# Performance work log

Hardware: AMD Instinct MI355X
Metric: run time of the kernel (lower is better)

Reference implementation:

```python
import jax, jax.numpy as jnp
import numpy as np

NEG_SLOPE = 0.01  # F.leaky_relu default
EPS = 1e-6


def setup_inputs() -> dict:
    key = jax.random.key(0)
    k1, k2, k3, k4 = jax.random.split(key, 4)
    N, E, IN, OUT = 100000, 1600000, 128, 64
    x = jax.random.normal(k1, (N, IN), dtype=jnp.float32)
    W = jax.random.normal(k2, (OUT, IN), dtype=jnp.float32) * (1.0 / np.sqrt(IN))
    a = jax.random.uniform(k3, (2 * OUT,), dtype=jnp.float32)  # uniform [0,1) as in init
    edge_index = jax.random.randint(k4, (2, E), 0, N, dtype=jnp.int64)
    return {"x": x, "W": W, "a": a, "edge_index": edge_index}


def reference(x, W, a, edge_index):
    N = x.shape[0]
    out_f = W.shape[0]
    # add self loops: append (i, i) for every node
    loops = jnp.arange(N, dtype=edge_index.dtype)
    ei = jnp.concatenate([edge_index, jnp.stack([loops, loops])], axis=1)
    src, dst = ei[0], ei[1]

    messages = x @ W.T                      # [N, out]
    h_src = messages[src]                   # [E', out]
    h_dst = messages[dst]                   # [E', out]

    # e = cat([h_dst, h_src]) . a  == h_dst.a[:out] + h_src.a[out:]
    e = h_dst @ a[:out_f] + h_src @ a[out_f:]
    e = jnp.where(e >= 0, e, NEG_SLOPE * e)  # leaky_relu
    w = jnp.exp(e)                           # unnormalized edge weights

    denom = jax.ops.segment_sum(w, dst, num_segments=N)                     # [N]
    agg = jax.ops.segment_sum(h_src * w[:, None], dst, num_segments=N)      # [N, out]
    return agg / jnp.clip(denom, EPS)[:, None]
```

## Files before the change

kernel.cpp:

```cpp
#include <hip/hip_runtime.h>
#include <hip/hip_bf16.h>

#define IN_F 128
#define OUT_F 64
#define NEG 0.01f
#define LDSP 132
#define WTP  68

#define BUCKET_N 256
#define EPB 8192
#define CAP 48
#define MAXB 512
#define MAXSLAB 512
#define CMAXIT 32

__device__ __forceinline__ float leaky_exp(float e) {
    e = (e >= 0.f) ? e : NEG * e;
    return expf(e);
}

__device__ __forceinline__ float b2f(unsigned int v) { return __uint_as_float(v); }

__global__ __launch_bounds__(256) void gemm_msg_kernel(
    const float* __restrict__ x, const float* __restrict__ W,
    const float* __restrict__ a,
    __hip_bfloat16* __restrict__ msg, float2* __restrict__ ab, int N)
{
    __shared__ float xs[64 * LDSP];
    __shared__ float Wt[IN_F * WTP];
    const int tid = threadIdx.x;
    const int base = blockIdx.x * 64;

#pragma unroll
    for (int t = 0; t < 8; ++t) {
        int i = tid + t * 256;
        int o = i & 63;
        int k4 = i >> 6;
        float4 wv = ((const float4*)W)[o * (IN_F / 4) + k4];
        Wt[(k4 * 4 + 0) * WTP + o] = wv.x;
        Wt[(k4 * 4 + 1) * WTP + o] = wv.y;
        Wt[(k4 * 4 + 2) * WTP + o] = wv.z;
        Wt[(k4 * 4 + 3) * WTP + o] = wv.w;
    }
#pragma unroll
    for (int t = 0; t < 8; ++t) {
        int i = tid + t * 256;
        int r = i >> 5, k4 = i & 31;
        int row = base + r;
        float4 xv = make_float4(0.f, 0.f, 0.f, 0.f);
        if (row < N) xv = ((const float4*)x)[(size_t)row * (IN_F / 4) + k4];
        *(float4*)&xs[r * LDSP + k4 * 4] = xv;
    }
    __syncthreads();

    const int tx = tid & 15;
    const int ty = tid >> 4;
    const float* xrow = &xs[(ty * 4) * LDSP];

    float acc[4][4] = {};
    for (int k = 0; k < IN_F; k += 4) {
        float xq[4][4], wq[4][4];
#pragma unroll
        for (int i = 0; i < 4; ++i)
            *(float4*)xq[i] = *(const float4*)&xrow[i * LDSP + k];
#pragma unroll
        for (int j = 0; j < 4; ++j)
            *(float4*)wq[j] = *(const float4*)&Wt[(k + j) * WTP + tx * 4];
#pragma unroll
        for (int ri = 0; ri < 4; ++ri)
#pragma unroll
            for (int ci = 0; ci < 4; ++ci) {
                acc[ri][ci] += xq[ri][0] * wq[0][ci];
                acc[ri][ci] += xq[ri][1] * wq[1][ci];
                acc[ri][ci] += xq[ri][2] * wq[2][ci];
                acc[ri][ci] += xq[ri][3] * wq[3][ci];
            }
    }

    float a_lo[4], a_hi[4];
#pragma unroll
    for (int ci = 0; ci < 4; ++ci) {
        a_lo[ci] = a[tx * 4 + ci];
        a_hi[ci] = a[OUT_F + tx * 4 + ci];
    }

#pragma unroll
    for (int ri = 0; ri < 4; ++ri) {
        int row = base + ty * 4 + ri;
        if (row < N) {
            union { ushort4 u; __hip_bfloat16 h[4]; } pk;
            pk.h[0] = __float2bfloat16(acc[ri][0]);
            pk.h[1] = __float2bfloat16(acc[ri][1]);
            pk.h[2] = __float2bfloat16(acc[ri][2]);
            pk.h[3] = __float2bfloat16(acc[ri][3]);
            *(ushort4*)&msg[(size_t)row * OUT_F + tx * 4] = pk.u;
        }
        float pa = acc[ri][0] * a_lo[0] + acc[ri][1] * a_lo[1] +
                   acc[ri][2] * a_lo[2] + acc[ri][3] * a_lo[3];
        float pb = acc[ri][0] * a_hi[0] + acc[ri][1] * a_hi[1] +
                   acc[ri][2] * a_hi[2] + acc[ri][3] * a_hi[3];
#pragma unroll
        for (int off = 1; off < 16; off <<= 1) {
            pa += __shfl_xor(pa, off);
            pb += __shfl_xor(pb, off);
        }
        if (tx == 0 && row < N) ab[row] = make_float2(pa, pb);
    }
}

__global__ __launch_bounds__(512) void partition_kernel(
    const int* __restrict__ src, const int* __restrict__ dst,
    int* __restrict__ counts, unsigned int* __restrict__ cells,
    int* __restrict__ bucket_tot, int E, int B, int NBLKP)
{
    __shared__ int cnt_s[MAXB];
    for (int i = threadIdx.x; i < B; i += 512) cnt_s[i] = 0;
    __syncthreads();

    const size_t pbase = (size_t)blockIdx.x * B;

#pragma unroll
    for (int u = 0; u < 4; ++u) {
        const int i4 = blockIdx.x * 2048 + u * 512 + threadIdx.x;
        const int e0 = i4 * 4;
        if (e0 + 3 < E) {
            int4 s4 = ((const int4*)src)[i4];
            int4 d4 = ((const int4*)dst)[i4];
            int b0 = d4.x >> 8, b1 = d4.y >> 8, b2 = d4.z >> 8, b3 = d4.w >> 8;
            int r0 = atomicAdd(&cnt_s[b0], 1);
            int r1 = atomicAdd(&cnt_s[b1], 1);
            int r2 = atomicAdd(&cnt_s[b2], 1);
            int r3 = atomicAdd(&cnt_s[b3], 1);
            if (r0 < CAP) cells[(pbase + b0) * CAP + r0] =
                (unsigned)s4.x | ((unsigned)(d4.x & 255) << 20);
            if (r1 < CAP) cells[(pbase + b1) * CAP + r1] =
                (unsigned)s4.y | ((unsigned)(d4.y & 255) << 20);
            if (r2 < CAP) cells[(pbase + b2) * CAP + r2] =
                (unsigned)s4.z | ((unsigned)(d4.z & 255) << 20);
            if (r3 < CAP) cells[(pbase + b3) * CAP + r3] =
                (unsigned)s4.w | ((unsigned)(d4.w & 255) << 20);
        } else {
            for (int e = e0; e < E && e < e0 + 4; ++e) {
                int s = src[e], d = dst[e];
                int b = d >> 8;
                int r = atomicAdd(&cnt_s[b], 1);
                if (r < CAP) cells[(pbase + b) * CAP + r] =
                    (unsigned)s | ((unsigned)(d & 255) << 20);
            }
        }
    }
    __syncthreads();
    for (int i = threadIdx.x; i < B; i += 512) {
        int c = min(cnt_s[i], CAP);
        counts[(size_t)i * NBLKP + blockIdx.x] = c;
        atomicAdd(&bucket_tot[i], c);
    }
}

__global__ __launch_bounds__(512) void bucket_scan_kernel(
    const int* __restrict__ bucket_tot, int* __restrict__ bucket_base,
    int* __restrict__ offs, int N, int B)
{
    __shared__ int tmp[512];
    const int t = threadIdx.x;
    int v = 0;
    if (t < B) {
        int nodes = N - t * BUCKET_N;
        nodes = max(0, min(BUCKET_N, nodes));
        v = bucket_tot[t] + nodes;
    }
    tmp[t] = v;
    __syncthreads();
#pragma unroll
    for (int d = 1; d < 512; d <<= 1) {
        int add = (t >= d) ? tmp[t - d] : 0;
        __syncthreads();
        tmp[t] += add;
        __syncthreads();
    }
    if (t < B) bucket_base[t] = tmp[t] - v;
    if (t == 511) offs[N] = tmp[511];
}

__global__ __launch_bounds__(512) void compact_kernel(
    const int* __restrict__ counts, const unsigned int* __restrict__ cells,
    const int* __restrict__ bucket_base, const float2* __restrict__ ab,
    int* __restrict__ offs, int2* __restrict__ edges,
    int N, int B, int NBLK, int NBLKP)
{
    __shared__ int cnt_l[MAXSLAB];
    __shared__ int hist[BUCKET_N];
    __shared__ int scan_s[BUCKET_N];
    __shared__ int cursor[BUCKET_N];
    __shared__ float alpha_s[BUCKET_N];
    const int b = blockIdx.x;
    const int tid = threadIdx.x;
    const int wave = tid >> 6, lane = tid & 63;

    for (int i = tid; i < NBLK; i += 512) cnt_l[i] = counts[(size_t)b * NBLKP + i];
    float2 myab = make_float2(0.f, 0.f);
    if (tid < BUCKET_N) {
        int g = b * BUCKET_N + tid;
        bool valid = (g < N);
        hist[tid] = valid ? 1 : 0;
        if (valid) myab = ab[g];
        alpha_s[tid] = myab.x;
    }
    __syncthreads();

    unsigned cell_c[CMAXIT];
#pragma unroll
    for (int it = 0; it < CMAXIT; ++it) {
        int sl = wave + it * 8;
        unsigned v = 0xFFFFFFFFu;
        if (sl < NBLK) {
            int c = cnt_l[sl];
            if (lane < c) {
                v = cells[((size_t)sl * B + b) * CAP + lane];
                atomicAdd(&hist[v >> 20], 1);
            }
        }
        cell_c[it] = v;
    }
    for (int sl = wave + CMAXIT * 8; sl < NBLK; sl += 8) {
        int c = cnt_l[sl];
        if (lane < c) {
            unsigned v = cells[((size_t)sl * B + b) * CAP + lane];
            atomicAdd(&hist[v >> 20], 1);
        }
    }
    __syncthreads();

    int hv = 0;
    if (tid < BUCKET_N) { hv = hist[tid]; scan_s[tid] = hv; }
    __syncthreads();
#pragma unroll
    for (int d = 1; d < BUCKET_N; d <<= 1) {
        int add = (tid < BUCKET_N && tid >= d) ? scan_s[tid - d] : 0;
        __syncthreads();
        if (tid < BUCKET_N) scan_s[tid] += add;
        __syncthreads();
    }
    const int gbase = bucket_base[b];
    if (tid < BUCKET_N) {
        int excl = scan_s[tid] - hv;
        int g = b * BUCKET_N + tid;
        if (g < N) {
            offs[g] = gbase + excl;
            float wself = leaky_exp(myab.x + myab.y);
            edges[gbase + excl] = make_int2(g, __float_as_int(wself));
            cursor[tid] = excl + 1;
        }
    }
    __syncthreads();

#pragma unroll
    for (int it = 0; it < CMAXIT; ++it) {
        unsigned v = cell_c[it];
        if (v != 0xFFFFFFFFu) {
            int s = v & 0xFFFFF;
            int l = (v >> 20) & 255;
            float w = leaky_exp(alpha_s[l] + ab[s].y);
            int pos = atomicAdd(&cursor[l], 1);
            edges[gbase + pos] = make_int2(s, __float_as_int(w));
        }
    }
    for (int sl = wave + CMAXIT * 8; sl < NBLK; sl += 8) {
        int c = cnt_l[sl];
        if (lane < c) {
            unsigned v = cells[((size_t)sl * B + b) * CAP + lane];
            int s = v & 0xFFFFF;
            int l = (v >> 20) & 255;
            float w = leaky_exp(alpha_s[l] + ab[s].y);
            int pos = atomicAdd(&cursor[l], 1);
            edges[gbase + pos] = make_int2(s, __float_as_int(w));
        }
    }
}

__global__ __launch_bounds__(256) void aggregate_kernel(
    const int* __restrict__ offs, const int2* __restrict__ edges,
    const __hip_bfloat16* __restrict__ msg,
    float* __restrict__ out, int N)
{
    const int node = blockIdx.x * 4 + (threadIdx.x >> 6);
    if (node >= N) return;
    const int lane = threadIdx.x & 63;
    const int g = lane & 15;
    const int u = lane >> 4;

    const unsigned short* msp = (const unsigned short*)msg;

    float acc0 = 0.f, acc1 = 0.f, acc2 = 0.f, acc3 = 0.f, den = 0.f;

    const int st = offs[node], en = offs[node + 1];

    int idx = st + u;
    int2 e = edges[min(idx, en - 1)];
    for (int j = st; j < en; j += 4) {
        const int nidx = idx + 4;
        const int2 enx = edges[min(nidx, en - 1)];
        const float w = (idx < en) ? __int_as_float(e.y) : 0.f;
        const ushort4 mv = *(const ushort4*)&msp[(size_t)e.x * OUT_F + 4 * g];
        acc0 += w * b2f((unsigned)mv.x << 16);
        acc1 += w * b2f((unsigned)mv.y << 16);
        acc2 += w * b2f((unsigned)mv.z << 16);
        acc3 += w * b2f((unsigned)mv.w << 16);
        den  += w;
        idx = nidx;
        e = enx;
    }

#pragma unroll
    for (int off = 16; off <= 32; off <<= 1) {
        acc0 += __shfl_xor(acc0, off);
        acc1 += __shfl_xor(acc1, off);
        acc2 += __shfl_xor(acc2, off);
        acc3 += __shfl_xor(acc3, off);
        den  += __shfl_xor(den, off);
    }

    if (lane < 16) {
        float dn = 1.f / fmaxf(den, 1e-6f);
        *(float4*)&out[(size_t)node * OUT_F + 4 * lane] =
            make_float4(acc0 * dn, acc1 * dn, acc2 * dn, acc3 * dn);
    }
}

extern "C" void kernel_launch(void* const* d_in, const int* in_sizes, int n_in,
                              void* d_out, int out_size, void* d_ws, size_t ws_size,
                              hipStream_t stream) {
    const float* x  = (const float*)d_in[0];
    const float* W  = (const float*)d_in[1];
    const float* a  = (const float*)d_in[2];
    const int*   ei = (const int*)d_in[3];
    float* out = (float*)d_out;

    const int IN = in_sizes[1] / OUT_F;
    const int N  = in_sizes[0] / IN;
    const int E  = in_sizes[3] / 2;
    const int B  = (N + BUCKET_N - 1) / BUCKET_N;
    const int NBLK  = (E + EPB - 1) / EPB;
    const int NBLKP = (NBLK + 3) & ~3;

    auto align16 = [](size_t v) { return (v + 15) & ~(size_t)15; };
    char* p = (char*)d_ws;
    __hip_bfloat16* msg = (__hip_bfloat16*)p; p += align16((size_t)N * OUT_F * 2);
    float2* ab    = (float2*)p; p += align16((size_t)N * 8);
    int*   counts = (int*)p;   p += align16((size_t)B * NBLKP * 4);
    unsigned int* cells = (unsigned int*)p; p += align16((size_t)NBLK * B * CAP * 4);
    int*   btot   = (int*)p;   p += align16((size_t)B * 4);
    int*   bbase  = (int*)p;   p += align16((size_t)B * 4);
    int*   offs   = (int*)p;   p += align16((size_t)(N + 1) * 4);
    int2*  edges  = (int2*)p;  p += align16((size_t)(E + N) * 8);

    const int* esrc = ei;
    const int* edst = ei + E;

    hipMemsetAsync(btot, 0, (size_t)B * 4, stream);

    gemm_msg_kernel<<<(N + 63) / 64, 256, 0, stream>>>(x, W, a, msg, ab, N);
    partition_kernel<<<NBLK, 512, 0, stream>>>(esrc, edst, counts, cells,
                                               btot, E, B, NBLKP);
    bucket_scan_kernel<<<1, 512, 0, stream>>>(btot, bbase, offs, N, B);
    compact_kernel<<<B, 512, 0, stream>>>(counts, cells, bbase, ab,
                                          offs, edges, N, B, NBLK, NBLKP);
    aggregate_kernel<<<(N + 3) / 4, 256, 0, stream>>>(offs, edges, msg, out, N);
}
```

Measured before the change: 152.6 us.

## Read x directly from global in GEMM and unroll aggregate edge loop by four

The GEMM kernel no longer stages the x tile in LDS. Each thread now reads its four x rows straight from global memory as float4 loads, which removes the large shared buffer and should allow more blocks per CU. The cost is uncoalesced, repeated global loads of x, since the 16 threads sharing a row group all read the same rows. The aggregate kernel now processes 16 edges per iteration, with four independent edge and message gathers in flight, replacing the one-ahead prefetch and adding a tail loop.

```diff
diff --git a/kernel.cpp b/kernel.cpp
--- a/kernel.cpp
+++ b/kernel.cpp
@@ -4,7 +4,6 @@
 #define IN_F 128
 #define OUT_F 64
 #define NEG 0.01f
-#define LDSP 132
 #define WTP  68
 
 #define BUCKET_N 256
@@ -26,7 +25,6 @@
     const float* __restrict__ a,
     __hip_bfloat16* __restrict__ msg, float2* __restrict__ ab, int N)
 {
-    __shared__ float xs[64 * LDSP];
     __shared__ float Wt[IN_F * WTP];
     const int tid = threadIdx.x;
     const int base = blockIdx.x * 64;
@@ -42,30 +40,28 @@
         Wt[(k4 * 4 + 2) * WTP + o] = wv.z;
         Wt[(k4 * 4 + 3) * WTP + o] = wv.w;
     }
-#pragma unroll
-    for (int t = 0; t < 8; ++t) {
-        int i = tid + t * 256;
-        int r = i >> 5, k4 = i & 31;
-        int row = base + r;
-        float4 xv = make_float4(0.f, 0.f, 0.f, 0.f);
-        if (row < N) xv = ((const float4*)x)[(size_t)row * (IN_F / 4) + k4];
-        *(float4*)&xs[r * LDSP + k4 * 4] = xv;
-    }
     __syncthreads();
 
     const int tx = tid & 15;
     const int ty = tid >> 4;
-    const float* xrow = &xs[(ty * 4) * LDSP];
+
+    const float4* xr[4];
+#pragma unroll
+    for (int ri = 0; ri < 4; ++ri) {
+        int row = min(base + ty * 4 + ri, N - 1);
+        xr[ri] = (const float4*)x + (size_t)row * (IN_F / 4);
+    }
 
     float acc[4][4] = {};
-    for (int k = 0; k < IN_F; k += 4) {
+#pragma unroll 4
+    for (int k4 = 0; k4 < IN_F / 4; ++k4) {
         float xq[4][4], wq[4][4];
 #pragma unroll
-        for (int i = 0; i < 4; ++i)
-            *(float4*)xq[i] = *(const float4*)&xrow[i * LDSP + k];
+        for (int ri = 0; ri < 4; ++ri)
+            *(float4*)xq[ri] = xr[ri][k4];
 #pragma unroll
         for (int j = 0; j < 4; ++j)
-            *(float4*)wq[j] = *(const float4*)&Wt[(k + j) * WTP + tx * 4];
+            *(float4*)wq[j] = *(const float4*)&Wt[(k4 * 4 + j) * WTP + tx * 4];
 #pragma unroll
         for (int ri = 0; ri < 4; ++ri)
 #pragma unroll
@@ -294,21 +290,35 @@
     float acc0 = 0.f, acc1 = 0.f, acc2 = 0.f, acc3 = 0.f, den = 0.f;
 
     const int st = offs[node], en = offs[node + 1];
+    const int deg = en - st;
 
     int idx = st + u;
-    int2 e = edges[min(idx, en - 1)];
-    for (int j = st; j < en; j += 4) {
-        const int nidx = idx + 4;
-        const int2 enx = edges[min(nidx, en - 1)];
-        const float w = (idx < en) ? __int_as_float(e.y) : 0.f;
-        const ushort4 mv = *(const ushort4*)&msp[(size_t)e.x * OUT_F + 4 * g];
+    int j = 0;
+    for (; j + 16 <= deg; j += 16) {
+#pragma unroll
+        for (int uu = 0; uu < 4; ++uu) {
+            int2 e = edges[idx + uu * 4];
+            float w = __int_as_float(e.y);
+            ushort4 mv = *(const ushort4*)&msp[(size_t)e.x * OUT_F + 4 * g];
+            acc0 += w * b2f((unsigned)mv.x << 16);
+            acc1 += w * b2f((unsigned)mv.y << 16);
+            acc2 += w * b2f((unsigned)mv.z << 16);
+            acc3 += w * b2f((unsigned)mv.w << 16);
+            den  += w;
+        }
+        idx += 16;
+    }
+    for (; j < deg; j += 4) {
+        int ii = min(idx, en - 1);
+        int2 e = edges[ii];
+        float w = (idx < en) ? __int_as_float(e.y) : 0.f;
+        ushort4 mv = *(const ushort4*)&msp[(size_t)e.x * OUT_F + 4 * g];
         acc0 += w * b2f((unsigned)mv.x << 16);
         acc1 += w * b2f((unsigned)mv.y << 16);
         acc2 += w * b2f((unsigned)mv.z << 16);
         acc3 += w * b2f((unsigned)mv.w << 16);
         den  += w;
-        idx = nidx;
-        e = enx;
+        idx += 4;
     }
 
 #pragma unroll
```

After: 141.0 us. -7.6%, faster.
